# Kernel optimization log

Hardware: AMD Instinct MI355X
Metric: run time of the kernel (lower is better)

Reference implementation:

```python
import jax, jax.numpy as jnp
import numpy as np

BN_EPS = 1e-5


def _batchnorm(x, gamma, beta):
    # training-mode BatchNorm2d: biased batch stats over (N, H, W)
    mean = jnp.mean(x, axis=(0, 2, 3), keepdims=True)
    var = jnp.var(x, axis=(0, 2, 3), keepdims=True)
    xn = (x - mean) * jax.lax.rsqrt(var + BN_EPS)
    return xn * gamma[None, :, None, None] + beta[None, :, None, None]


def _bin_weight(w):
    # BitConv2d_Robust: w_bin = sign(w) * mean(|w|) per output channel (STE in fwd is just the value)
    alpha = jnp.mean(jnp.abs(w), axis=(1, 2, 3), keepdims=True)
    return jax.lax.stop_gradient(jnp.sign(w) * alpha - w) + w


def _conv(x, w, b, pad):
    y = jax.lax.conv_general_dilated(
        x, w, window_strides=(1, 1), padding=[(pad, pad), (pad, pad)],
        dimension_numbers=('NCHW', 'OIHW', 'NCHW'))
    return y + b[None, :, None, None]


def setup_inputs() -> dict:
    key = jax.random.key(0)
    ks = jax.random.split(key, 14)
    B, Cin, Cout, T, H, W = 16, 128, 256, 512, 64, 64
    fan1 = Cin * 9
    fan2 = Cout * 9
    return {
        'x': jax.random.normal(ks[0], (B, Cin, H, W), jnp.float32),
        't': jax.random.normal(ks[1], (B, T), jnp.float32),
        'bn1_g': jnp.ones((Cin,), jnp.float32),
        'bn1_b': jnp.zeros((Cin,), jnp.float32),
        'w1': jax.random.normal(ks[2], (Cout, Cin, 3, 3), jnp.float32) / np.sqrt(fan1),
        'b1': jax.random.normal(ks[3], (Cout,), jnp.float32) * 0.01,
        'tW': jax.random.normal(ks[4], (Cout, T), jnp.float32) / np.sqrt(T),
        'tb': jax.random.normal(ks[5], (Cout,), jnp.float32) * 0.01,
        'bn2_g': jnp.ones((Cout,), jnp.float32),
        'bn2_b': jnp.zeros((Cout,), jnp.float32),
        'w2': jax.random.normal(ks[6], (Cout, Cout, 3, 3), jnp.float32) / np.sqrt(fan2),
        'b2': jax.random.normal(ks[7], (Cout,), jnp.float32) * 0.01,
        'ws': jax.random.normal(ks[8], (Cout, Cin, 1, 1), jnp.float32) / np.sqrt(Cin),
        'bs': jax.random.normal(ks[9], (Cout,), jnp.float32) * 0.01,
    }


def reference(x, t, bn1_g, bn1_b, w1, b1, tW, tb, bn2_g, bn2_b, w2, b2, ws, bs):
    h = jnp.sign(_batchnorm(x, bn1_g, bn1_b))                # BN + sign binarize
    h = _conv(h, _bin_weight(w1), b1, pad=1)                  # binarized 3x3 conv
    temb = t @ tW.T + tb                                      # time MLP -> [B, Cout]
    h = h + temb[:, :, None, None]
    h = jnp.sign(_batchnorm(h, bn2_g, bn2_b))
    h = _conv(h, _bin_weight(w2), b2, pad=1)
    skip = _conv(x, _bin_weight(ws), bs, pad=0)               # 1x1 binarized skip (in_ch != out_ch)
    return h + skip
```

## Files before the change

kernel.cpp:

```cpp
#include <hip/hip_runtime.h>
#include <stdint.h>

typedef unsigned int uint;
typedef short bf16x8 __attribute__((ext_vector_type(8)));
typedef float f32x4 __attribute__((ext_vector_type(4)));

#define EPS 1e-5f


__global__ __launch_bounds__(256) void k_bn1_part(const float* __restrict__ x, float* __restrict__ part) {
  int c = blockIdx.x, chunk = blockIdx.y;
  float s = 0.f, s2 = 0.f;
  #pragma unroll
  for (int jb = 0; jb < 2; ++jb) {
    int b = chunk * 2 + jb;
    const float4* xb = (const float4*)(x + (((size_t)((b << 7) | c)) << 12));
    #pragma unroll
    for (int k = 0; k < 4; ++k) {
      float4 q = xb[k * 256 + threadIdx.x];
      s += (q.x + q.y) + (q.z + q.w);
      s2 += q.x * q.x + q.y * q.y + q.z * q.z + q.w * q.w;
    }
  }
  #pragma unroll
  for (int off = 32; off > 0; off >>= 1) { s += __shfl_down(s, off); s2 += __shfl_down(s2, off); }
  __shared__ float ls[4], ls2[4];
  int wid = threadIdx.x >> 6, lane = threadIdx.x & 63;
  if (lane == 0) { ls[wid] = s; ls2[wid] = s2; }
  __syncthreads();
  if (threadIdx.x == 0) {
    part[(c * 8 + chunk) * 2 + 0] = ls[0] + ls[1] + ls[2] + ls[3];
    part[(c * 8 + chunk) * 2 + 1] = ls2[0] + ls2[1] + ls2[2] + ls2[3];
  }
}

__global__ void k_bn1_fin(const float* __restrict__ part, const float* __restrict__ g,
                          const float* __restrict__ be, float* __restrict__ sc, float* __restrict__ sh) {
  int c = threadIdx.x;
  float s = 0.f, s2 = 0.f;
  for (int k = 0; k < 8; ++k) { s += part[(c * 8 + k) * 2]; s2 += part[(c * 8 + k) * 2 + 1]; }
  const float inv = 1.f / 65536.f;
  float m = s * inv, var = s2 * inv - m * m;
  float rs = rsqrtf(var + EPS);
  float scale = rs * g[c];
  sc[c] = scale;
  sh[c] = be[c] - m * scale;
}

__global__ __launch_bounds__(128) void k_packw1(const float* __restrict__ w1, uint* __restrict__ wb,
                                                float* __restrict__ alpha, ushort* __restrict__ wT1) {
  int co = blockIdx.x, wid = threadIdx.x >> 6, lane = threadIdx.x & 63;
  int ci = threadIdx.x;
  const float* wp = w1 + (co * 128 + ci) * 9;
  float wv[9]; float s = 0.f;
  #pragma unroll
  for (int tp = 0; tp < 9; ++tp) { wv[tp] = wp[tp]; s += fabsf(wv[tp]); }
  #pragma unroll
  for (int tp = 0; tp < 9; ++tp) {
    wT1[(((tp << 2) + (ci >> 5)) << 13) + (co << 5) + (ci & 31)] = (wv[tp] > 0.f) ? 0x3F80u : 0xBF80u;
    unsigned long long m = __ballot(wv[tp] > 0.f);
    if (lane == 0) {
      wb[(co * 9 + tp) * 4 + wid * 2 + 0] = (uint)m;
      wb[(co * 9 + tp) * 4 + wid * 2 + 1] = (uint)(m >> 32);
    }
  }
  #pragma unroll
  for (int off = 32; off > 0; off >>= 1) s += __shfl_down(s, off);
  __shared__ float l2[2];
  if (lane == 0) l2[wid] = s;
  __syncthreads();
  if (threadIdx.x == 0) alpha[co] = (l2[0] + l2[1]) * (1.f / 1152.f);
}

__global__ __launch_bounds__(256) void k_packw2(const float* __restrict__ w2, uint* __restrict__ wb,
                                                float* __restrict__ alpha, ushort* __restrict__ wT) {
  int co = blockIdx.x, wid = threadIdx.x >> 6, lane = threadIdx.x & 63;
  int ci = threadIdx.x;
  const float* wp = w2 + (co * 256 + ci) * 9;
  float wv[9]; float s = 0.f;
  #pragma unroll
  for (int tp = 0; tp < 9; ++tp) { wv[tp] = wp[tp]; s += fabsf(wv[tp]); }
  int chunk = ci >> 7, kc = (ci >> 5) & 3, cil = ci & 31;
  #pragma unroll
  for (int tp = 0; tp < 9; ++tp) {
    wT[(((tp << 3) + (chunk << 2) + kc) << 13) + (co << 5) + cil] = (wv[tp] > 0.f) ? 0x3F80u : 0xBF80u;
    unsigned long long m = __ballot(wv[tp] > 0.f);
    if (lane == 0) {
      wb[(co * 9 + tp) * 8 + wid * 2 + 0] = (uint)m;
      wb[(co * 9 + tp) * 8 + wid * 2 + 1] = (uint)(m >> 32);
    }
  }
  #pragma unroll
  for (int off = 32; off > 0; off >>= 1) s += __shfl_down(s, off);
  __shared__ float l4[4];
  if (lane == 0) l4[wid] = s;
  __syncthreads();
  if (threadIdx.x == 0) alpha[co] = (l4[0] + l4[1] + l4[2] + l4[3]) * (1.f / 2304.f);
}

__global__ __launch_bounds__(256) void k_base(const uint* __restrict__ wb1, const uint* __restrict__ wb2,
                                              int* __restrict__ base1, int* __restrict__ base2) {
  int co = threadIdx.x;
  int pc1[9], pc2[9];
  #pragma unroll
  for (int tp = 0; tp < 9; ++tp) {
    uint a = 0;
    #pragma unroll
    for (int k = 0; k < 4; ++k) a += __popc(wb1[co * 36 + tp * 4 + k]);
    pc1[tp] = (int)a;
    uint b = 0;
    #pragma unroll
    for (int k = 0; k < 8; ++k) b += __popc(wb2[co * 72 + tp * 8 + k]);
    pc2[tp] = (int)b;
  }
  #pragma unroll
  for (int pat = 0; pat < 9; ++pat) {
    int yt = pat / 3, xt = pat % 3;
    int b1v = 1152, b2v = 2304;
    #pragma unroll
    for (int tp = 0; tp < 9; ++tp) {
      int dy = tp / 3 - 1, dx = tp % 3 - 1;
      bool inv = (dy < 0 && yt == 0) || (dy > 0 && yt == 2) || (dx < 0 && xt == 0) || (dx > 0 && xt == 2);
      if (inv) { b1v -= 128 - 2 * pc1[tp]; b2v -= 256 - 2 * pc2[tp]; }
    }
    base1[pat * 256 + co] = b1v;
    base2[pat * 256 + co] = b2v;
  }
}

__global__ __launch_bounds__(128) void k_packws(const float* __restrict__ wsk, float* __restrict__ swT) {
  int co = blockIdx.x, ci = threadIdx.x;
  float v = wsk[co * 128 + ci];
  float s = fabsf(v);
  #pragma unroll
  for (int off = 32; off > 0; off >>= 1) s += __shfl_down(s, off);
  __shared__ float l2[2]; __shared__ float tot;
  int wid = threadIdx.x >> 6, lane = threadIdx.x & 63;
  if (lane == 0) l2[wid] = s;
  __syncthreads();
  if (threadIdx.x == 0) tot = (l2[0] + l2[1]) * (1.f / 128.f);
  __syncthreads();
  float a = tot;
  swT[ci * 256 + co] = (v > 0.f) ? a : -a;
}

__global__ __launch_bounds__(256) void k_temb(const float* __restrict__ t, const float* __restrict__ tW,
                                              const float* __restrict__ tbias, float* __restrict__ temb) {
  int b = blockIdx.x, co = threadIdx.x;
  const float* tr = t + b * 512;
  const float* wr = tW + co * 512;
  float a0 = 0, a1 = 0, a2 = 0, a3 = 0;
  #pragma unroll 8
  for (int k = 0; k < 512; k += 4) {
    a0 = fmaf(tr[k + 0], wr[k + 0], a0);
    a1 = fmaf(tr[k + 1], wr[k + 1], a1);
    a2 = fmaf(tr[k + 2], wr[k + 2], a2);
    a3 = fmaf(tr[k + 3], wr[k + 3], a3);
  }
  temb[b * 256 + co] = (a0 + a1) + (a2 + a3) + tbias[co];
}

__global__ __launch_bounds__(256, 2) void k_skip(const float* __restrict__ x, const float* __restrict__ swT,
                                                 const float* __restrict__ bsk, const float* __restrict__ b2,
                                                 const float* __restrict__ sc1, const float* __restrict__ sh1,
                                                 uint* __restrict__ sbinw, ushort* __restrict__ h1w,
                                                 int mfma1, float* __restrict__ out) {
  __shared__ float xs[128 * 64];
  __shared__ float wsl[128 * 64];
  int g = blockIdx.x;
  int b = g >> 6;
  int px0 = (g & 63) << 6;
  int co0 = blockIdx.y << 6;
  int t = threadIdx.x;

  {
    const float* xb = x + ((size_t)(b << 7) << 12) + px0;
    float4* xs4 = (float4*)xs;
    #pragma unroll
    for (int k = 0; k < 8; ++k) {
      int idx = k * 256 + t;
      int ci = idx >> 4, f4 = idx & 15;
      xs4[idx] = *(const float4*)(xb + ((size_t)ci << 12) + (f4 << 2));
    }
  }
  {
    float4* ws4 = (float4*)wsl;
    #pragma unroll
    for (int k = 0; k < 8; ++k) {
      int idx = k * 256 + t;
      int ci = idx >> 4, f4 = idx & 15;
      ws4[idx] = *(const float4*)(swT + ci * 256 + co0 + (f4 << 2));
    }
  }
  __syncthreads();

  if (blockIdx.y == 0) {
    int px = t & 63, wd = t >> 6;
    int ci0 = wd << 5;
    if (mfma1) {
      ushort hv[32];
      #pragma unroll
      for (int i = 0; i < 32; ++i) {
        int ci = ci0 + i;
        float v = xs[ci * 64 + px];
        hv[i] = ((v * sc1[ci] + sh1[ci]) > 0.f) ? (ushort)0x3F80u : (ushort)0xBF80u;
      }
      uint4* dst = (uint4*)(h1w + (((size_t)((b << 12) | (px0 + px))) << 7) + (wd << 5));
      const uint4* src = (const uint4*)hv;
      dst[0] = src[0]; dst[1] = src[1]; dst[2] = src[2]; dst[3] = src[3];
    } else {
      uint acc = 0;
      #pragma unroll
      for (int i = 0; i < 32; ++i) {
        int ci = ci0 + i;
        float v = xs[ci * 64 + px];
        acc |= ((v * sc1[ci] + sh1[ci]) > 0.f ? 1u : 0u) << i;
      }
      sbinw[(((size_t)b << 12) | (px0 + px)) * 4 + wd] = acc;
    }
  }

  int tx = t & 15, ty = t >> 4;
  const float4* xs4 = (const float4*)xs;
  const float4* ws4 = (const float4*)wsl;
  float4 acc0 = make_float4(0, 0, 0, 0), acc1 = acc0, acc2 = acc0, acc3 = acc0;
  #pragma unroll 4
  for (int ci = 0; ci < 128; ++ci) {
    float4 xv = xs4[ci * 16 + tx];
    float4 wv = ws4[ci * 16 + ty];
    acc0.x = fmaf(wv.x, xv.x, acc0.x); acc0.y = fmaf(wv.x, xv.y, acc0.y);
    acc0.z = fmaf(wv.x, xv.z, acc0.z); acc0.w = fmaf(wv.x, xv.w, acc0.w);
    acc1.x = fmaf(wv.y, xv.x, acc1.x); acc1.y = fmaf(wv.y, xv.y, acc1.y);
    acc1.z = fmaf(wv.y, xv.z, acc1.z); acc1.w = fmaf(wv.y, xv.w, acc1.w);
    acc2.x = fmaf(wv.z, xv.x, acc2.x); acc2.y = fmaf(wv.z, xv.y, acc2.y);
    acc2.z = fmaf(wv.z, xv.z, acc2.z); acc2.w = fmaf(wv.z, xv.w, acc2.w);
    acc3.x = fmaf(wv.w, xv.x, acc3.x); acc3.y = fmaf(wv.w, xv.y, acc3.y);
    acc3.z = fmaf(wv.w, xv.z, acc3.z); acc3.w = fmaf(wv.w, xv.w, acc3.w);
  }

  float* op = out + ((size_t)b << 20) + px0 + (tx << 2);
  int cob = co0 + (ty << 2);
  float4 r;
  r = acc0; { float bb = bsk[cob + 0] + b2[cob + 0]; r.x += bb; r.y += bb; r.z += bb; r.w += bb; }
  *(float4*)(op + (size_t)(cob + 0) * 4096) = r;
  r = acc1; { float bb = bsk[cob + 1] + b2[cob + 1]; r.x += bb; r.y += bb; r.z += bb; r.w += bb; }
  *(float4*)(op + (size_t)(cob + 1) * 4096) = r;
  r = acc2; { float bb = bsk[cob + 2] + b2[cob + 2]; r.x += bb; r.y += bb; r.z += bb; r.w += bb; }
  *(float4*)(op + (size_t)(cob + 2) * 4096) = r;
  r = acc3; { float bb = bsk[cob + 3] + b2[cob + 3]; r.x += bb; r.y += bb; r.z += bb; r.w += bb; }
  *(float4*)(op + (size_t)(cob + 3) * 4096) = r;
}

__global__ __launch_bounds__(256, 2) void k_conv1_mfma(const ushort* __restrict__ h1,
                                                       const ushort* __restrict__ wT1,
                                                       short* __restrict__ S1,
                                                       float* __restrict__ part_s,
                                                       float* __restrict__ part_s2) {
  __shared__ ushort act[4 * 66 * 128];
  int bidx = blockIdx.x;
  int s = (bidx & 7) * 64 + (bidx >> 3);
  int b = s >> 5, y0 = (s & 31) << 1;
  int lane = threadIdx.x & 63, wave = threadIdx.x >> 6;
  int co0 = wave << 6;
  int l15 = lane & 15, lk = lane >> 4;

  f32x4 acc[4][8] = {};
  const uint4* h1g = (const uint4*)h1;
  uint4* a4 = (uint4*)act;
  const size_t abase = (size_t)((co0 + l15) << 5) + (lk << 3);

#define LOADAV(dst, ptr)                                                     \
  {                                                                          \
    _Pragma("unroll")                                                        \
    for (int ct_ = 0; ct_ < 4; ++ct_)                                        \
      dst[ct_] = *(const bf16x8*)((ptr) + abase + (ct_ << 9));               \
  }
#define KC_BLOCK(AV, kcv)                                                    \
  {                                                                          \
    _Pragma("unroll")                                                        \
    for (int r_ = 0; r_ < 2; ++r_) {                                         \
      bf16x8 Bv[4];                                                          \
      _Pragma("unroll")                                                      \
      for (int pt_ = 0; pt_ < 4; ++pt_) {                                    \
        int xi_ = (r_ + ty) * 66 + tx + pt_ * 16 + l15;                      \
        int u_ = (((xi_ << 4) + ((kcv) << 2) + lk) ^ (xi_ & 7));             \
        Bv[pt_] = *(bf16x8*)&act[u_ << 3];                                   \
      }                                                                      \
      _Pragma("unroll")                                                      \
      for (int ct_ = 0; ct_ < 4; ++ct_)                                      \
        _Pragma("unroll")                                                    \
        for (int pt_ = 0; pt_ < 4; ++pt_)                                    \
          acc[ct_][r_ * 4 + pt_] = __builtin_amdgcn_mfma_f32_16x16x32_bf16(  \
              AV[ct_], Bv[pt_], acc[ct_][r_ * 4 + pt_], 0, 0, 0);            \
    }                                                                        \
  }

  #pragma unroll 1
  for (int i = 0; i < 17; ++i) {
    int idx = i * 256 + threadIdx.x;
    if (idx < 4224) {
      int q = idx & 15, rowxz = idx >> 4;
      int xz = rowxz % 66, r = rowxz / 66;
      int yy = y0 + r - 1, xx = xz - 1;
      uint4 v = make_uint4(0, 0, 0, 0);
      if (((unsigned)yy < 64u) && ((unsigned)xx < 64u))
        v = h1g[(size_t)((b << 12) | (yy << 6) | xx) * 16 + q];
      a4[((rowxz << 4) + q) ^ (rowxz & 7)] = v;
    }
  }
  __syncthreads();

  bf16x8 AvA[4], AvB[4];
  LOADAV(AvA, wT1);
  #pragma unroll 1
  for (int tp = 0; tp < 9; ++tp) {
    int ty = tp / 3, tx = tp % 3;
    const ushort* wtp = wT1 + ((size_t)tp << 15);
    const ushort* wnx = (tp < 8) ? (wtp + (1 << 15)) : wtp;

    LOADAV(AvB, wtp + (1 << 13));  KC_BLOCK(AvA, 0);
    LOADAV(AvA, wtp + (2 << 13));  KC_BLOCK(AvB, 1);
    LOADAV(AvB, wtp + (3 << 13));  KC_BLOCK(AvA, 2);
    LOADAV(AvA, wnx);              KC_BLOCK(AvB, 3);
  }
#undef LOADAV
#undef KC_BLOCK

  #pragma unroll
  for (int ct = 0; ct < 4; ++ct)
    #pragma unroll
    for (int r = 0; r < 2; ++r)
      #pragma unroll
      for (int pt = 0; pt < 4; ++pt) {
        int x = pt * 16 + l15;
        short* ob = S1 + ((size_t)b << 20) + ((y0 + r) << 6) + x;
        #pragma unroll
        for (int j = 0; j < 4; ++j) {
          int co = co0 + ct * 16 + lk * 4 + j;
          ob[(size_t)co << 12] = (short)acc[ct][r * 4 + pt][j];
        }
      }
  #pragma unroll
  for (int ct = 0; ct < 4; ++ct) {
    float s1v[4] = {0, 0, 0, 0}, s2v[4] = {0, 0, 0, 0};
    #pragma unroll
    for (int k = 0; k < 8; ++k)
      #pragma unroll
      for (int j = 0; j < 4; ++j) {
        float v = acc[ct][k][j];
        s1v[j] += v; s2v[j] += v * v;
      }
    #pragma unroll
    for (int off = 1; off < 16; off <<= 1)
      #pragma unroll
      for (int j = 0; j < 4; ++j) {
        s1v[j] += __shfl_xor(s1v[j], off);
        s2v[j] += __shfl_xor(s2v[j], off);
      }
    if (l15 == 0) {
      #pragma unroll
      for (int j = 0; j < 4; ++j) {
        int co = co0 + ct * 16 + lk * 4 + j;
        part_s[(size_t)s * 256 + co] = s1v[j];
        part_s2[(size_t)s * 256 + co] = s2v[j];
      }
    }
  }
}

__global__ void k_bn2_fin2(const float* __restrict__ part_s, const float* __restrict__ part_s2,
                           const float* __restrict__ al1, const float* __restrict__ b1,
                           const float* __restrict__ g2, const float* __restrict__ be2,
                           const float* __restrict__ temb,
                           float* __restrict__ A, float* __restrict__ Bc, float* __restrict__ Cc) {
  int co = blockIdx.x;
  int t = threadIdx.x;
  float sS = 0.f, scS = 0.f, s2 = 0.f;
  for (int k = 0; k < 8; ++k) {
    int blk = t + k * 64;
    int b = blk >> 5;
    float c = b1[co] + temb[(b << 8) + co];
    float Sv = part_s[(size_t)blk * 256 + co];
    sS += Sv; scS += c * Sv; s2 += part_s2[(size_t)blk * 256 + co];
  }
  #pragma unroll
  for (int off = 32; off > 0; off >>= 1) {
    sS += __shfl_down(sS, off); scS += __shfl_down(scS, off); s2 += __shfl_down(s2, off);
  }
  if (t == 0) {
    float a = al1[co];
    float sumc = 0.f, sumc2 = 0.f;
    for (int b = 0; b < 16; ++b) { float c = b1[co] + temb[(b << 8) + co]; sumc += c; sumc2 += c * c; }
    float sumY = a * sS + 4096.f * sumc;
    float sumY2 = a * a * s2 + 2.f * a * scS + 4096.f * sumc2;
    const float inv = 1.f / 65536.f;
    float m = sumY * inv, var = sumY2 * inv - m * m;
    float rs = rsqrtf(var + EPS);
    float gg = rs * g2[co];
    A[co] = a * gg;
    Bc[co] = (b1[co] - m) * gg + be2[co];
    Cc[co] = gg;
  }
}

__global__ __launch_bounds__(256, 1) void k_conv1(const uint4* __restrict__ sbin, const uint* __restrict__ wb1,
                                                  const int* __restrict__ base1, short* __restrict__ S1) {
  __shared__ uint wlds[32 * 36];
  __shared__ int blds[9 * 32];
  int co0 = blockIdx.y << 5;
  #pragma unroll
  for (int k = 0; k < 4; ++k) wlds[k * 256 + threadIdx.x] = wb1[co0 * 36 + k * 256 + threadIdx.x];
  if (threadIdx.x < 128) wlds[1024 + threadIdx.x] = wb1[co0 * 36 + 1024 + threadIdx.x];
  #pragma unroll
  for (int k = 0; k < 2; ++k) {
    int idx = k * 256 + threadIdx.x;
    if (idx < 288) blds[idx] = base1[(idx >> 5) * 256 + co0 + (idx & 31)];
  }
  int bt = blockIdx.x;
  int b = bt >> 4;
  int y = ((bt & 15) << 2) | (threadIdx.x >> 6);
  int cx = threadIdx.x & 63;
  uint nb[9][4];
  #pragma unroll
  for (int dy = -1; dy <= 1; ++dy)
    #pragma unroll
    for (int dx = -1; dx <= 1; ++dx) {
      int tp = (dy + 1) * 3 + (dx + 1);
      int yy = y + dy, xx = cx + dx;
      bool v = ((unsigned)yy < 64u) && ((unsigned)xx < 64u);
      uint4 q = make_uint4(0, 0, 0, 0);
      if (v) q = sbin[(b << 12) | (yy << 6) | xx];
      nb[tp][0] = q.x; nb[tp][1] = q.y; nb[tp][2] = q.z; nb[tp][3] = q.w;
    }
  int pat = ((y == 0) ? 0 : ((y == 63) ? 6 : 3)) + ((cx == 0) ? 0 : ((cx == 63) ? 2 : 1));
  __syncthreads();
  int p = (y << 6) | cx;
  short* op = S1 + ((size_t)b << 20) + ((size_t)co0 << 12) + p;
  #pragma unroll 1
  for (int cc = 0; cc < 4; ++cc) {
    short accv[8];
    #pragma unroll
    for (int j = 0; j < 8; ++j) {
      int co_l = cc * 8 + j;
      const uint4* wp4 = (const uint4*)(wlds + co_l * 36);
      uint m0 = 0, m1 = 0, m2 = 0, m3 = 0;
      #pragma unroll
      for (int tp = 0; tp < 9; ++tp) {
        uint4 w4 = wp4[tp];
        m0 += __popc(nb[tp][0] ^ w4.x);
        m1 += __popc(nb[tp][1] ^ w4.y);
        m2 += __popc(nb[tp][2] ^ w4.z);
        m3 += __popc(nb[tp][3] ^ w4.w);
      }
      accv[j] = (short)(blds[pat * 32 + co_l] - 2 * (int)((m0 + m1) + (m2 + m3)));
    }
    #pragma unroll
    for (int j = 0; j < 8; ++j) op[(size_t)(cc * 8 + j) << 12] = accv[j];
  }
}

__global__ __launch_bounds__(256) void k_bn2_part(const short* __restrict__ S1, const float* __restrict__ al1,
                                                  const float* __restrict__ b1, const float* __restrict__ temb,
                                                  float* __restrict__ part) {
  int co = blockIdx.x, chunk = blockIdx.y;
  float a = al1[co], bb = b1[co];
  float s = 0.f, s2 = 0.f;
  #pragma unroll
  for (int jb = 0; jb < 2; ++jb) {
    int b = chunk * 2 + jb;
    float tb_ = bb + temb[(b << 8) | co];
    const uint4* sp = (const uint4*)(S1 + ((size_t)b << 20) + ((size_t)co << 12));
    #pragma unroll
    for (int k = 0; k < 2; ++k) {
      uint4 q = sp[k * 256 + threadIdx.x];
      uint ws[4] = {q.x, q.y, q.z, q.w};
      #pragma unroll
      for (int w = 0; w < 4; ++w) {
        float f0 = fmaf(a, (float)((short)(ws[w] & 0xffffu)), tb_);
        float f1 = fmaf(a, (float)((short)(ws[w] >> 16)), tb_);
        s += f0 + f1;
        s2 += f0 * f0 + f1 * f1;
      }
    }
  }
  #pragma unroll
  for (int off = 32; off > 0; off >>= 1) { s += __shfl_down(s, off); s2 += __shfl_down(s2, off); }
  __shared__ float ls[4], ls2[4];
  int wid = threadIdx.x >> 6, lane = threadIdx.x & 63;
  if (lane == 0) { ls[wid] = s; ls2[wid] = s2; }
  __syncthreads();
  if (threadIdx.x == 0) {
    part[(co * 8 + chunk) * 2 + 0] = ls[0] + ls[1] + ls[2] + ls[3];
    part[(co * 8 + chunk) * 2 + 1] = ls2[0] + ls2[1] + ls2[2] + ls2[3];
  }
}

__global__ void k_bn2_fin(const float* __restrict__ part, const float* __restrict__ al1,
                          const float* __restrict__ b1, const float* __restrict__ g2,
                          const float* __restrict__ be2, float* __restrict__ A,
                          float* __restrict__ Bc, float* __restrict__ Cc) {
  int co = threadIdx.x;
  float s = 0.f, s2 = 0.f;
  for (int k = 0; k < 8; ++k) { s += part[(co * 8 + k) * 2]; s2 += part[(co * 8 + k) * 2 + 1]; }
  const float inv = 1.f / 65536.f;
  float m = s * inv, var = s2 * inv - m * m;
  float rs = rsqrtf(var + EPS);
  float gg = rs * g2[co];
  A[co] = al1[co] * gg;
  Bc[co] = (b1[co] - m) * gg + be2[co];
  Cc[co] = gg;
}

__global__ __launch_bounds__(256) void k_bin2_bf16(const short* __restrict__ S1, const float* __restrict__ A,
                                                   const float* __restrict__ Bc, const float* __restrict__ Cc,
                                                   const float* __restrict__ temb, uint4* __restrict__ h2u4) {
  __shared__ uint4 tile[64 * 32];
  int b = blockIdx.x >> 6;
  int px0 = (blockIdx.x & 63) << 6;
  int pxl = threadIdx.x & 63, quad = threadIdx.x >> 6;
  const short* sp = S1 + ((size_t)b << 20) + (px0 + pxl);
  const float* tp = temb + (b << 8);
  #pragma unroll 1
  for (int g = 0; g < 8; ++g) {
    uint d[4];
    #pragma unroll
    for (int h = 0; h < 4; ++h) {
      int c0 = quad * 64 + g * 8 + h * 2;
      float v0 = A[c0] * (float)sp[(size_t)c0 << 12] + Bc[c0] + Cc[c0] * tp[c0];
      float v1 = A[c0 + 1] * (float)sp[(size_t)(c0 + 1) << 12] + Bc[c0 + 1] + Cc[c0 + 1] * tp[c0 + 1];
      uint s0 = (v0 > 0.f) ? 0x3F80u : 0xBF80u;
      uint s1 = (v1 > 0.f) ? 0x3F80u : 0xBF80u;
      d[h] = s0 | (s1 << 16);
    }
    int slot = quad * 8 + g;
    tile[pxl * 32 + (slot ^ (pxl & 7))] = make_uint4(d[0], d[1], d[2], d[3]);
  }
  __syncthreads();
  uint4* dst = h2u4 + ((size_t)(b << 12) + px0) * 32;
  #pragma unroll
  for (int k = 0; k < 8; ++k) {
    int c = k * 256 + threadIdx.x;
    int px = c >> 5, slot = c & 31;
    dst[c] = tile[px * 32 + (slot ^ (px & 7))];
  }
}

__global__ __launch_bounds__(256, 2) void k_conv2_mfma(const ushort* __restrict__ h2,
                                                       const ushort* __restrict__ wT,
                                                       const float* __restrict__ al2,
                                                       float* __restrict__ out) {
  __shared__ ushort act[4 * 66 * 128];
  int bidx = blockIdx.x;
  int s = (bidx & 7) * 64 + (bidx >> 3);
  int b = s >> 5, y0 = (s & 31) << 1;
  int lane = threadIdx.x & 63, wave = threadIdx.x >> 6;
  int co0 = wave << 6;
  int l15 = lane & 15, lk = lane >> 4;

  f32x4 acc[4][8] = {};
  const uint4* h2g = (const uint4*)h2;
  uint4* a4 = (uint4*)act;
  const size_t abase = (size_t)((co0 + l15) << 5) + (lk << 3);

#define LOADAV(dst, ptr)                                                     \
  {                                                                          \
    _Pragma("unroll")                                                        \
    for (int ct_ = 0; ct_ < 4; ++ct_)                                        \
      dst[ct_] = *(const bf16x8*)((ptr) + abase + (ct_ << 9));               \
  }
#define KC_BLOCK(AV, kcv)                                                    \
  {                                                                          \
    _Pragma("unroll")                                                        \
    for (int r_ = 0; r_ < 2; ++r_) {                                         \
      bf16x8 Bv[4];                                                          \
      _Pragma("unroll")                                                      \
      for (int pt_ = 0; pt_ < 4; ++pt_) {                                    \
        int xi_ = (r_ + ty) * 66 + tx + pt_ * 16 + l15;                      \
        int u_ = (((xi_ << 4) + ((kcv) << 2) + lk) ^ (xi_ & 7));             \
        Bv[pt_] = *(bf16x8*)&act[u_ << 3];                                   \
      }                                                                      \
      _Pragma("unroll")                                                      \
      for (int ct_ = 0; ct_ < 4; ++ct_)                                      \
        _Pragma("unroll")                                                    \
        for (int pt_ = 0; pt_ < 4; ++pt_)                                    \
          acc[ct_][r_ * 4 + pt_] = __builtin_amdgcn_mfma_f32_16x16x32_bf16(  \
              AV[ct_], Bv[pt_], acc[ct_][r_ * 4 + pt_], 0, 0, 0);            \
    }                                                                        \
  }

  #pragma unroll 1
  for (int chunk = 0; chunk < 2; ++chunk) {
    if (chunk) __syncthreads();
    #pragma unroll 1
    for (int i = 0; i < 17; ++i) {
      int idx = i * 256 + threadIdx.x;
      if (idx < 4224) {
        int q = idx & 15, rowxz = idx >> 4;
        int xz = rowxz % 66, r = rowxz / 66;
        int yy = y0 + r - 1, xx = xz - 1;
        uint4 v = make_uint4(0, 0, 0, 0);
        if (((unsigned)yy < 64u) && ((unsigned)xx < 64u))
          v = h2g[(size_t)((b << 12) | (yy << 6) | xx) * 32 + chunk * 16 + q];
        a4[((rowxz << 4) + q) ^ (rowxz & 7)] = v;
      }
    }
    __syncthreads();

    const ushort* wch = wT + ((size_t)chunk << 15);
    bf16x8 AvA[4], AvB[4];
    LOADAV(AvA, wch);

    #pragma unroll 1
    for (int tp = 0; tp < 9; ++tp) {
      int ty = tp / 3, tx = tp % 3;
      const ushort* wtp = wch + ((size_t)tp << 16);
      const ushort* wnx = (tp < 8) ? (wtp + (1 << 16)) : wtp;

      LOADAV(AvB, wtp + (1 << 13));  KC_BLOCK(AvA, 0);
      LOADAV(AvA, wtp + (2 << 13));  KC_BLOCK(AvB, 1);
      LOADAV(AvB, wtp + (3 << 13));  KC_BLOCK(AvA, 2);
      LOADAV(AvA, wnx);              KC_BLOCK(AvB, 3);
    }
  }
#undef LOADAV
#undef KC_BLOCK

  #pragma unroll
  for (int ct = 0; ct < 4; ++ct) {
    #pragma unroll
    for (int r = 0; r < 2; ++r) {
      #pragma unroll
      for (int pt = 0; pt < 4; ++pt) {
        int x = pt * 16 + l15;
        float* ob = out + ((size_t)b << 20) + ((y0 + r) << 6) + x;
        #pragma unroll
        for (int j = 0; j < 4; ++j) {
          int co = co0 + ct * 16 + lk * 4 + j;
          float* p = ob + ((size_t)co << 12);
          *p = fmaf(al2[co], acc[ct][r * 4 + pt][j], *p);
        }
      }
    }
  }
}

__global__ __launch_bounds__(256) void k_bin2_packed(const short* __restrict__ S1, const float* __restrict__ A,
                                                     const float* __restrict__ Bc, const float* __restrict__ Cc,
                                                     const float* __restrict__ temb, uint4* __restrict__ hbin) {
  int pg = blockIdx.x * 256 + threadIdx.x;
  int b = pg >> 12, p = pg & 4095;
  int c0 = blockIdx.y << 7;
  const short* sp = S1 + ((size_t)b << 20) + p;
  const float* tp = temb + (b << 8);
  uint w[4];
  #pragma unroll
  for (int wd = 0; wd < 4; ++wd) {
    uint acc = 0;
    #pragma unroll
    for (int i = 0; i < 32; ++i) {
      int co = c0 + wd * 32 + i;
      float v = A[co] * (float)sp[(size_t)co << 12] + Bc[co] + Cc[co] * tp[co];
      acc |= (v > 0.f ? 1u : 0u) << i;
    }
    w[wd] = acc;
  }
  hbin[pg * 2 + blockIdx.y] = make_uint4(w[0], w[1], w[2], w[3]);
}

__global__ __launch_bounds__(256, 1) void k_conv2_pop(const uint4* __restrict__ hbin, const uint* __restrict__ wb2,
                                                      const int* __restrict__ base2, const float* __restrict__ al2,
                                                      float* __restrict__ out) {
  __shared__ uint wlds[32 * 72];
  __shared__ int blds[9 * 32];
  int co0 = blockIdx.y << 5;
  #pragma unroll
  for (int k = 0; k < 9; ++k) wlds[k * 256 + threadIdx.x] = wb2[co0 * 72 + k * 256 + threadIdx.x];
  #pragma unroll
  for (int k = 0; k < 2; ++k) {
    int idx = k * 256 + threadIdx.x;
    if (idx < 288) blds[idx] = base2[(idx >> 5) * 256 + co0 + (idx & 31)];
  }
  int bt = blockIdx.x;
  int b = bt >> 4;
  int y = ((bt & 15) << 2) | (threadIdx.x >> 6);
  int cx = threadIdx.x & 63;
  uint nb[9][8];
  #pragma unroll
  for (int dy = -1; dy <= 1; ++dy)
    #pragma unroll
    for (int dx = -1; dx <= 1; ++dx) {
      int tp = (dy + 1) * 3 + (dx + 1);
      int yy = y + dy, xx = cx + dx;
      bool v = ((unsigned)yy < 64u) && ((unsigned)xx < 64u);
      uint4 q0 = make_uint4(0, 0, 0, 0), q1 = make_uint4(0, 0, 0, 0);
      if (v) {
        int pix = (b << 12) | (yy << 6) | xx;
        q0 = hbin[pix * 2 + 0];
        q1 = hbin[pix * 2 + 1];
      }
      nb[tp][0] = q0.x; nb[tp][1] = q0.y; nb[tp][2] = q0.z; nb[tp][3] = q0.w;
      nb[tp][4] = q1.x; nb[tp][5] = q1.y; nb[tp][6] = q1.z; nb[tp][7] = q1.w;
    }
  int pat = ((y == 0) ? 0 : ((y == 63) ? 6 : 3)) + ((cx == 0) ? 0 : ((cx == 63) ? 2 : 1));
  __syncthreads();
  int p = (y << 6) | cx;
  float* op = out + ((size_t)b << 20) + ((size_t)co0 << 12) + p;
  #pragma unroll 1
  for (int cc = 0; cc < 4; ++cc) {
    float ov[8];
    #pragma unroll
    for (int j = 0; j < 8; ++j) ov[j] = op[(size_t)(cc * 8 + j) << 12];
    #pragma unroll
    for (int j = 0; j < 8; ++j) {
      int co_l = cc * 8 + j;
      const uint4* wp4 = (const uint4*)(wlds + co_l * 72);
      uint m0 = 0, m1 = 0, m2 = 0, m3 = 0;
      #pragma unroll
      for (int tp = 0; tp < 9; ++tp) {
        uint4 wa = wp4[tp * 2 + 0];
        uint4 wb_ = wp4[tp * 2 + 1];
        m0 += __popc(nb[tp][0] ^ wa.x);
        m1 += __popc(nb[tp][1] ^ wa.y);
        m2 += __popc(nb[tp][2] ^ wa.z);
        m3 += __popc(nb[tp][3] ^ wa.w);
        m0 += __popc(nb[tp][4] ^ wb_.x);
        m1 += __popc(nb[tp][5] ^ wb_.y);
        m2 += __popc(nb[tp][6] ^ wb_.z);
        m3 += __popc(nb[tp][7] ^ wb_.w);
      }
      int acc = blds[pat * 32 + co_l] - 2 * (int)((m0 + m1) + (m2 + m3));
      ov[j] = fmaf(al2[co0 + co_l], (float)acc, ov[j]);
    }
    #pragma unroll
    for (int j = 0; j < 8; ++j) op[(size_t)(cc * 8 + j) << 12] = ov[j];
  }
}

extern "C" void kernel_launch(void* const* d_in, const int* in_sizes, int n_in,
                              void* d_out, int out_size, void* d_ws, size_t ws_size,
                              hipStream_t stream) {
  const float* x    = (const float*)d_in[0];
  const float* t    = (const float*)d_in[1];
  const float* bn1g = (const float*)d_in[2];
  const float* bn1b = (const float*)d_in[3];
  const float* w1   = (const float*)d_in[4];
  const float* b1   = (const float*)d_in[5];
  const float* tW   = (const float*)d_in[6];
  const float* tb   = (const float*)d_in[7];
  const float* bn2g = (const float*)d_in[8];
  const float* bn2b = (const float*)d_in[9];
  const float* w2   = (const float*)d_in[10];
  const float* b2   = (const float*)d_in[11];
  const float* wsk  = (const float*)d_in[12];
  const float* bsk  = (const float*)d_in[13];
  float* out = (float*)d_out;
  char* ws = (char*)d_ws;

  float* bn1part = (float*)(ws + 0);
  float* sc1     = (float*)(ws + 8192);
  float* sh1     = (float*)(ws + 8704);
  uint4* sbin    = (uint4*)(ws + 9216);
  uint*  wb1     = (uint*) (ws + 1057792);
  float* al1     = (float*)(ws + 1094656);
  uint*  wb2     = (uint*) (ws + 1095680);
  float* al2     = (float*)(ws + 1169408);
  float* swkT    = (float*)(ws + 1170432);
  float* temb    = (float*)(ws + 1301504);
  float* bn2part = (float*)(ws + 1317888);
  float* A2      = (float*)(ws + 1334272);
  float* Bc2     = (float*)(ws + 1335296);
  float* Cc2     = (float*)(ws + 1336320);
  int*   base1g  = (int*)  (ws + 1337344);
  int*   base2g  = (int*)  (ws + 1346560);
  uint4*  hbin    = (uint4*)(ws + 1355776);
  float*  part_s  = (float*)(ws + 1355776);
  float*  part_s2 = (float*)(ws + 1880064);
  ushort* wT1     = (ushort*)(ws + 2404352);
  ushort* wT2     = (ushort*)(ws + 3452928);
  short*  S1      = (short*)(ws + 4632576);
  ushort* h2      = (ushort*)(ws + 38187008);
  ushort* h1      = (ushort*)(ws + 71741440);
  const size_t WS_NEED2 = 71741440ULL;
  const size_t WS_NEED1 = 88518656ULL;
  bool mode2 = (ws_size >= WS_NEED2);
  bool mode1 = (ws_size >= WS_NEED1);

  k_bn1_part<<<dim3(128, 8), 256, 0, stream>>>(x, bn1part);
  k_bn1_fin<<<1, 128, 0, stream>>>(bn1part, bn1g, bn1b, sc1, sh1);
  k_packw1<<<256, 128, 0, stream>>>(w1, wb1, al1, wT1);
  k_packw2<<<256, 256, 0, stream>>>(w2, wb2, al2, wT2);
  k_base<<<1, 256, 0, stream>>>(wb1, wb2, base1g, base2g);
  k_packws<<<256, 128, 0, stream>>>(wsk, swkT);
  k_temb<<<16, 256, 0, stream>>>(t, tW, tb, temb);
  k_skip<<<dim3(1024, 4), 256, 0, stream>>>(x, swkT, bsk, b2, sc1, sh1, (uint*)sbin, h1,
                                            mode1 ? 1 : 0, out);
  if (mode1) {
    k_conv1_mfma<<<512, 256, 0, stream>>>(h1, wT1, S1, part_s, part_s2);
    k_bn2_fin2<<<256, 64, 0, stream>>>(part_s, part_s2, al1, b1, bn2g, bn2b, temb, A2, Bc2, Cc2);
  } else {
    k_conv1<<<dim3(256, 8), 256, 0, stream>>>(sbin, wb1, base1g, S1);
    k_bn2_part<<<dim3(256, 8), 256, 0, stream>>>(S1, al1, b1, temb, bn2part);
    k_bn2_fin<<<1, 256, 0, stream>>>(bn2part, al1, b1, bn2g, bn2b, A2, Bc2, Cc2);
  }
  if (mode2) {
    k_bin2_bf16<<<1024, 256, 0, stream>>>(S1, A2, Bc2, Cc2, temb, (uint4*)h2);
    k_conv2_mfma<<<512, 256, 0, stream>>>(h2, wT2, al2, out);
  } else {
    k_bin2_packed<<<dim3(256, 2), 256, 0, stream>>>(S1, A2, Bc2, Cc2, temb, hbin);
    k_conv2_pop<<<dim3(256, 8), 256, 0, stream>>>(hbin, wb2, base2g, al2, out);
  }
}
```

Before: 231.7 us.

## Enlarge skip-conv tile to 128x128 with K-chunked padded shared memory

The 1x1 skip conv kernel now computes a 128-pixel by 128-channel tile per block, with an 8x8 register micro-tile per thread, instead of 64x64 with 4x4. Input channels are streamed in four chunks of 32 through padded shared buffers, and the BN1 sign packing is done per chunk. This cuts how often x is re-read from global memory across output-channel blocks (2 instead of 4) and raises FMA work per shared-memory load. In exchange the grid shrinks to 1024 blocks, there is more register pressure, and only half the threads do the binarize step.

Result: no change. 227.2 us (median of 3 runs) (-1.9%).

```diff
diff --git a/kernel.cpp b/kernel.cpp
--- a/kernel.cpp
+++ b/kernel.cpp
@@ -165,90 +165,98 @@
                                                  const float* __restrict__ sc1, const float* __restrict__ sh1,
                                                  uint* __restrict__ sbinw, ushort* __restrict__ h1w,
                                                  int mfma1, float* __restrict__ out) {
-  __shared__ float xs[128 * 64];
-  __shared__ float wsl[128 * 64];
-  int g = blockIdx.x;
-  int b = g >> 6;
-  int px0 = (g & 63) << 6;
-  int co0 = blockIdx.y << 6;
+  __shared__ float xs[32 * 136];
+  __shared__ float wsl[32 * 128];
+  int s = blockIdx.x;
+  int b = s >> 5;
+  int px0 = (s & 31) << 7;
+  int co0 = blockIdx.y << 7;
   int t = threadIdx.x;
-
-  {
-    const float* xb = x + ((size_t)(b << 7) << 12) + px0;
-    float4* xs4 = (float4*)xs;
-    #pragma unroll
-    for (int k = 0; k < 8; ++k) {
-      int idx = k * 256 + t;
-      int ci = idx >> 4, f4 = idx & 15;
-      xs4[idx] = *(const float4*)(xb + ((size_t)ci << 12) + (f4 << 2));
-    }
-  }
-  {
-    float4* ws4 = (float4*)wsl;
-    #pragma unroll
-    for (int k = 0; k < 8; ++k) {
-      int idx = k * 256 + t;
-      int ci = idx >> 4, f4 = idx & 15;
-      ws4[idx] = *(const float4*)(swT + ci * 256 + co0 + (f4 << 2));
-    }
-  }
-  __syncthreads();
-
-  if (blockIdx.y == 0) {
-    int px = t & 63, wd = t >> 6;
-    int ci0 = wd << 5;
-    if (mfma1) {
-      ushort hv[32];
+  int tx = t & 15, ty = t >> 4;
+
+  float4 acc[8][2];
+  #pragma unroll
+  for (int i = 0; i < 8; ++i) { acc[i][0] = make_float4(0, 0, 0, 0); acc[i][1] = make_float4(0, 0, 0, 0); }
+
+  #pragma unroll 1
+  for (int kc = 0; kc < 4; ++kc) {
+    if (kc) __syncthreads();
+    #pragma unroll
+    for (int k2 = 0; k2 < 4; ++k2) {
+      int idx = k2 * 256 + t;
+      int ci_l = idx >> 5, pxl = (idx & 31) << 2;
+      float4 v = *(const float4*)(x + (((size_t)((b << 7) | (kc * 32 + ci_l))) << 12) + px0 + pxl);
+      int g = pxl >> 3;
+      *(float4*)&xs[ci_l * 136 + g * 8 + ((g >> 2) << 1) + (pxl & 7)] = v;
+    }
+    #pragma unroll
+    for (int k2 = 0; k2 < 4; ++k2) {
+      int idx = k2 * 256 + t;
+      int ci_l = idx >> 5, col = (idx & 31) << 2;
+      *(float4*)&wsl[ci_l * 128 + col] = *(const float4*)(swT + (size_t)(kc * 32 + ci_l) * 256 + co0 + col);
+    }
+    __syncthreads();
+
+    if (blockIdx.y == 0 && t < 128) {
+      int pxl = t;
+      int g = pxl >> 3;
+      int xo = g * 8 + ((g >> 2) << 1) + (pxl & 7);
+      if (mfma1) {
+        ushort hv[32];
+        #pragma unroll
+        for (int i = 0; i < 32; ++i) {
+          int ci = kc * 32 + i;
+          float v = xs[i * 136 + xo];
+          hv[i] = ((v * sc1[ci] + sh1[ci]) > 0.f) ? (ushort)0x3F80u : (ushort)0xBF80u;
+        }
+        uint4* dst = (uint4*)(h1w + (((size_t)((b << 12) | (px0 + pxl))) << 7) + (kc << 5));
+        const uint4* srcv = (const uint4*)hv;
+        dst[0] = srcv[0]; dst[1] = srcv[1]; dst[2] = srcv[2]; dst[3] = srcv[3];
+      } else {
+        uint accb = 0;
+        #pragma unroll
+        for (int i = 0; i < 32; ++i) {
+          int ci = kc * 32 + i;
+          float v = xs[i * 136 + xo];
+          accb |= ((v * sc1[ci] + sh1[ci]) > 0.f ? 1u : 0u) << i;
+        }
+        sbinw[(((size_t)b << 12) | (px0 + pxl)) * 4 + kc] = accb;
+      }
+    }
+
+    int xbase = tx * 8 + ((tx >> 2) << 1);
+    int wbase = ty * 8;
+    #pragma unroll 2
+    for (int ci = 0; ci < 32; ++ci) {
+      float4 xv0 = *(float4*)&xs[ci * 136 + xbase];
+      float4 xv1 = *(float4*)&xs[ci * 136 + xbase + 4];
+      float4 wv0 = *(float4*)&wsl[ci * 128 + wbase];
+      float4 wv1 = *(float4*)&wsl[ci * 128 + wbase + 4];
+      float wq[8] = {wv0.x, wv0.y, wv0.z, wv0.w, wv1.x, wv1.y, wv1.z, wv1.w};
       #pragma unroll
-      for (int i = 0; i < 32; ++i) {
-        int ci = ci0 + i;
-        float v = xs[ci * 64 + px];
-        hv[i] = ((v * sc1[ci] + sh1[ci]) > 0.f) ? (ushort)0x3F80u : (ushort)0xBF80u;
-      }
-      uint4* dst = (uint4*)(h1w + (((size_t)((b << 12) | (px0 + px))) << 7) + (wd << 5));
-      const uint4* src = (const uint4*)hv;
-      dst[0] = src[0]; dst[1] = src[1]; dst[2] = src[2]; dst[3] = src[3];
-    } else {
-      uint acc = 0;
-      #pragma unroll
-      for (int i = 0; i < 32; ++i) {
-        int ci = ci0 + i;
-        float v = xs[ci * 64 + px];
-        acc |= ((v * sc1[ci] + sh1[ci]) > 0.f ? 1u : 0u) << i;
-      }
-      sbinw[(((size_t)b << 12) | (px0 + px)) * 4 + wd] = acc;
-    }
-  }
-
-  int tx = t & 15, ty = t >> 4;
-  const float4* xs4 = (const float4*)xs;
-  const float4* ws4 = (const float4*)wsl;
-  float4 acc0 = make_float4(0, 0, 0, 0), acc1 = acc0, acc2 = acc0, acc3 = acc0;
-  #pragma unroll 4
-  for (int ci = 0; ci < 128; ++ci) {
-    float4 xv = xs4[ci * 16 + tx];
-    float4 wv = ws4[ci * 16 + ty];
-    acc0.x = fmaf(wv.x, xv.x, acc0.x); acc0.y = fmaf(wv.x, xv.y, acc0.y);
-    acc0.z = fmaf(wv.x, xv.z, acc0.z); acc0.w = fmaf(wv.x, xv.w, acc0.w);
-    acc1.x = fmaf(wv.y, xv.x, acc1.x); acc1.y = fmaf(wv.y, xv.y, acc1.y);
-    acc1.z = fmaf(wv.y, xv.z, acc1.z); acc1.w = fmaf(wv.y, xv.w, acc1.w);
-    acc2.x = fmaf(wv.z, xv.x, acc2.x); acc2.y = fmaf(wv.z, xv.y, acc2.y);
-    acc2.z = fmaf(wv.z, xv.z, acc2.z); acc2.w = fmaf(wv.z, xv.w, acc2.w);
-    acc3.x = fmaf(wv.w, xv.x, acc3.x); acc3.y = fmaf(wv.w, xv.y, acc3.y);
-    acc3.z = fmaf(wv.w, xv.z, acc3.z); acc3.w = fmaf(wv.w, xv.w, acc3.w);
-  }
-
-  float* op = out + ((size_t)b << 20) + px0 + (tx << 2);
-  int cob = co0 + (ty << 2);
-  float4 r;
-  r = acc0; { float bb = bsk[cob + 0] + b2[cob + 0]; r.x += bb; r.y += bb; r.z += bb; r.w += bb; }
-  *(float4*)(op + (size_t)(cob + 0) * 4096) = r;
-  r = acc1; { float bb = bsk[cob + 1] + b2[cob + 1]; r.x += bb; r.y += bb; r.z += bb; r.w += bb; }
-  *(float4*)(op + (size_t)(cob + 1) * 4096) = r;
-  r = acc2; { float bb = bsk[cob + 2] + b2[cob + 2]; r.x += bb; r.y += bb; r.z += bb; r.w += bb; }
-  *(float4*)(op + (size_t)(cob + 2) * 4096) = r;
-  r = acc3; { float bb = bsk[cob + 3] + b2[cob + 3]; r.x += bb; r.y += bb; r.z += bb; r.w += bb; }
-  *(float4*)(op + (size_t)(cob + 3) * 4096) = r;
+      for (int i = 0; i < 8; ++i) {
+        acc[i][0].x = fmaf(wq[i], xv0.x, acc[i][0].x);
+        acc[i][0].y = fmaf(wq[i], xv0.y, acc[i][0].y);
+        acc[i][0].z = fmaf(wq[i], xv0.z, acc[i][0].z);
+        acc[i][0].w = fmaf(wq[i], xv0.w, acc[i][0].w);
+        acc[i][1].x = fmaf(wq[i], xv1.x, acc[i][1].x);
+        acc[i][1].y = fmaf(wq[i], xv1.y, acc[i][1].y);
+        acc[i][1].z = fmaf(wq[i], xv1.z, acc[i][1].z);
+        acc[i][1].w = fmaf(wq[i], xv1.w, acc[i][1].w);
+      }
+    }
+  }
+
+  float* ob = out + ((size_t)b << 20) + px0 + tx * 8;
+  #pragma unroll
+  for (int i = 0; i < 8; ++i) {
+    int co = co0 + ty * 8 + i;
+    float bb = bsk[co] + b2[co];
+    float4 r0 = acc[i][0]; r0.x += bb; r0.y += bb; r0.z += bb; r0.w += bb;
+    float4 r1 = acc[i][1]; r1.x += bb; r1.y += bb; r1.z += bb; r1.w += bb;
+    *(float4*)(ob + ((size_t)co << 12)) = r0;
+    *(float4*)(ob + ((size_t)co << 12) + 4) = r1;
+  }
 }
 
 __global__ __launch_bounds__(256, 2) void k_conv1_mfma(const ushort* __restrict__ h1,
@@ -792,8 +800,8 @@
   k_base<<<1, 256, 0, stream>>>(wb1, wb2, base1g, base2g);
   k_packws<<<256, 128, 0, stream>>>(wsk, swkT);
   k_temb<<<16, 256, 0, stream>>>(t, tW, tb, temb);
-  k_skip<<<dim3(1024, 4), 256, 0, stream>>>(x, swkT, bsk, b2, sc1, sh1, (uint*)sbin, h1,
-                                            mode1 ? 1 : 0, out);
+  k_skip<<<dim3(512, 2), 256, 0, stream>>>(x, swkT, bsk, b2, sc1, sh1, (uint*)sbin, h1,
+                                           mode1 ? 1 : 0, out);
   if (mode1) {
     k_conv1_mfma<<<512, 256, 0, stream>>>(h1, wT1, S1, part_s, part_s2);
     k_bn2_fin2<<<256, 64, 0, stream>>>(part_s, part_s2, al1, b1, bn2g, bn2b, temb, A2, Bc2, Cc2);
```
